# Kernel tuning notes

Measured on AMD Instinct MI355X. Metric: run time of the kernel, lower is better.

Reference implementation:

```python
import jax, jax.numpy as jnp
import numpy as np

B, C, H, W = 4, 256, 64, 64


def conv_bn_relu(x, w, b):
    # 3x3 conv, stride 1, pad 1 (SAME) + folded eval-mode BatchNorm (absorbed
    # into w, b as a per-channel affine) + ReLU.
    y = jax.lax.conv_general_dilated(
        x, w, window_strides=(1, 1), padding='SAME',
        dimension_numbers=('NCHW', 'OIHW', 'NCHW'))
    return jax.nn.relu(y + b[None, :, None, None])


def setup_inputs() -> dict:
    key = jax.random.key(0)
    ks = jax.random.split(key, 9)

    def wgt(k):
        return (jax.random.normal(k, (C, C, 3, 3), jnp.float32) * 0.02)

    def bias(k):
        return (jax.random.normal(jax.random.fold_in(k, 1), (C,), jnp.float32) * 0.02)

    return {
        'x': jax.random.normal(ks[0], (B, C, H, W), jnp.float32),
        'wq': wgt(ks[1]), 'bq': bias(ks[1]),
        'wk': wgt(ks[2]), 'bk': bias(ks[2]),
        'wv': wgt(ks[3]), 'bv': bias(ks[3]),
        'wo': wgt(ks[4]), 'bo': bias(ks[4]),
    }


def reference(x, wq, bq, wk, bk, wv, bv, wo, bo):
    b, c, h, w = x.shape
    n = h * w
    # gen_attmap: conv-BN-ReLU projections, flatten spatial dims
    q = conv_bn_relu(x, wq, bq).reshape(b, c, n)   # [B, C, N]
    k = conv_bn_relu(x, wk, bk).reshape(b, c, n)   # [B, C, N]
    v = conv_bn_relu(x, wv, bv).reshape(b, c, n)   # [B, C, N]
    # sim_map = softmax(Q^T K) over keys; context = sim_map @ V^T
    sim = jax.nn.softmax(jnp.einsum('bcn,bcm->bnm', q, k), axis=-1)  # [B, N, N]
    ctx = jnp.einsum('bnm,bcm->bcn', sim, v).reshape(b, c, h, w)
    # sub_factor == 1: the block-rearranged branch and the avg-pooled branch
    # are identical (rearrange, avgpool(1,1) and interpolate(scale=1) are all
    # identity), so x_div + x_avg == 2 * ctx.
    return conv_bn_relu(ctx + ctx, wo, bo)
```

## Files before the change

### kernel.cpp

```cpp
#include <hip/hip_runtime.h>
#include <hip/hip_fp16.h>
#include <math.h>

#define NN 4096
#define CC 256

typedef __attribute__((ext_vector_type(8))) short bf16x8;
typedef __attribute__((ext_vector_type(8))) _Float16 f16x8;
typedef __attribute__((ext_vector_type(4))) float f32x4;
typedef __attribute__((ext_vector_type(16))) float f32x16;
typedef __attribute__((ext_vector_type(8))) unsigned short u16x8;
typedef __attribute__((ext_vector_type(4))) unsigned short u16x4;
typedef __attribute__((ext_vector_type(4))) unsigned int u32x4;

__device__ inline unsigned short f2bf(float f) {
  unsigned u = __float_as_uint(f);
  return (unsigned short)((u + 0x7FFFu + ((u >> 16) & 1u)) >> 16);
}
__device__ inline float bf2f(unsigned short u) {
  return __uint_as_float(((unsigned)u) << 16);
}
__device__ inline unsigned short f2h(float f) {
  __half h = __float2half(f);
  return static_cast<__half_raw>(h).x;
}

__device__ inline void gload16(const void* g, void* l) {
  __builtin_amdgcn_global_load_lds(
      (const __attribute__((address_space(1))) void*)g,
      (__attribute__((address_space(3))) void*)l, 16, 0, 0);
}

__global__ __launch_bounds__(256) void prep_w(
    const float* __restrict__ w0, const float* __restrict__ w1,
    const float* __restrict__ w2, const float* __restrict__ w3,
    unsigned short* __restrict__ wT2, unsigned short* __restrict__ zp)
{
  int bx = blockIdx.x;
  int widx = bx >> 8;
  const float* src = (widx == 0) ? w0 : (widx == 1) ? w1 : (widx == 2) ? w2 : w3;
  int p = ((bx & 255) << 8) + threadIdx.x;
  unsigned short* dst = wT2 + (size_t)widx * 589824;
  const float* s9 = src + (size_t)p * 9;
#pragma unroll
  for (int s = 0; s < 9; ++s) dst[(size_t)s * 65536 + p] = f2bf(s9[s]);
  if (bx == 0 && threadIdx.x < 128) zp[threadIdx.x] = 0;
}

__global__ __launch_bounds__(256) void prep_x(
    const float* __restrict__ x, unsigned short* __restrict__ xT)
{
  __shared__ unsigned short T[64][72];
  int tid = threadIdx.x, bx = blockIdx.x;
  int b = bx >> 8, c0 = ((bx >> 6) & 3) * 64, n0 = (bx & 63) * 64;
#pragma unroll
  for (int it = 0; it < 16; ++it) {
    int c_l = (tid >> 6) + it * 4;
    int n_l = tid & 63;
    T[n_l][c_l] = f2bf(x[((size_t)(b * 256 + c0 + c_l)) * 4096 + n0 + n_l]);
  }
  __syncthreads();
#pragma unroll
  for (int it = 0; it < 8; ++it) {
    int n_l = (tid >> 5) + it * 8;
    int cp = (tid & 31) * 2;
    unsigned v = (unsigned)T[n_l][cp] | ((unsigned)T[n_l][cp + 1] << 16);
    *(unsigned*)&xT[((size_t)(b * 4096 + n0 + n_l)) * 256 + c0 + cp] = v;
  }
}

__global__ __launch_bounds__(256) void conv_mfma(
    const unsigned short* __restrict__ A,
    const unsigned short* __restrict__ W,
    const float* __restrict__ bias,
    void* __restrict__ out, int mode,
    const unsigned short* __restrict__ zp)
{
  __shared__ unsigned short As[2][128 * 64];
  __shared__ unsigned short Bs[2][64 * 64];

  const int tid = threadIdx.x;
  const int lane = tid & 63;
  const int w = tid >> 6;
  const int wr = w >> 1, wc = w & 1;
  const int nt = blockIdx.x & 3;
  const int mt = blockIdx.x >> 2;
  const int m0 = mt * 128;
  const int co0 = nt * 64;

  const int aslot = (lane & 7) ^ (lane >> 3);
  int gmj[4], yj[4], xj[4];
#pragma unroll
  for (int j = 0; j < 4; ++j) {
    int row = w * 32 + j * 8 + (lane >> 3);
    int gm = m0 + row;
    gmj[j] = gm;
    int n = gm & (NN - 1);
    yj[j] = n >> 6;
    xj[j] = n & 63;
  }
  int browj[2];
#pragma unroll
  for (int j = 0; j < 2; ++j)
    browj[j] = co0 + w * 16 + j * 8 + (lane >> 3);

  f32x4 acc[4][2];
#pragma unroll
  for (int mi = 0; mi < 4; ++mi)
#pragma unroll
    for (int ni = 0; ni < 2; ++ni) acc[mi][ni] = (f32x4){0.f, 0.f, 0.f, 0.f};

  auto stage = [&](int step, int sb) {
    int s = step >> 2, t = step & 3;
    int dy = s / 3 - 1, dx = s - (s / 3) * 3 - 1;
    const unsigned short* abase = A + t * 64 + aslot * 8;
    const unsigned short* wbase = W + ((size_t)s << 16) + t * 64 + aslot * 8;
#pragma unroll
    for (int j = 0; j < 4; ++j) {
      int yy = yj[j] + dy, xx = xj[j] + dx;
      bool valid = ((unsigned)yy < 64u) && ((unsigned)xx < 64u);
      const void* ga = valid
          ? (const void*)(abase + (size_t)(gmj[j] + dy * 64 + dx) * 256)
          : (const void*)zp;
      gload16(ga, (void*)&As[sb][(w * 4 + j) * 512]);
    }
#pragma unroll
    for (int j = 0; j < 2; ++j) {
      const void* gb = (const void*)(wbase + (size_t)browj[j] * 256);
      gload16(gb, (void*)&Bs[sb][(w * 2 + j) * 512]);
    }
  };

  const int r = lane & 15;
  const int klane = lane >> 4;
  const int rs = r & 7;

  int buf = 0;
  stage(0, 0);
  __syncthreads();
  for (int step = 0; step < 36; ++step) {
    if (step + 1 < 36) stage(step + 1, buf ^ 1);
    const unsigned short* as = As[buf];
    const unsigned short* bs = Bs[buf];
#pragma unroll
    for (int kk = 0; kk < 2; ++kk) {
      int slot = (kk * 4 + klane) ^ rs;
      bf16x8 a[4], bq[2];
#pragma unroll
      for (int mi = 0; mi < 4; ++mi)
        a[mi] = *(const bf16x8*)&as[(wr * 64 + mi * 16 + r) * 64 + slot * 8];
#pragma unroll
      for (int ni = 0; ni < 2; ++ni)
        bq[ni] = *(const bf16x8*)&bs[(wc * 32 + ni * 16 + r) * 64 + slot * 8];
#pragma unroll
      for (int mi = 0; mi < 4; ++mi)
#pragma unroll
        for (int ni = 0; ni < 2; ++ni)
          acc[mi][ni] = __builtin_amdgcn_mfma_f32_16x16x32_bf16(
              a[mi], bq[ni], acc[mi][ni], 0, 0, 0);
    }
    __syncthreads();
    buf ^= 1;
  }

  const int r4 = lane >> 4;
  const int colb = lane & 15;
  if (mode == 0) {
    unsigned short* o16 = (unsigned short*)out;
#pragma unroll
    for (int ni = 0; ni < 2; ++ni) {
      int co = co0 + wc * 32 + ni * 16 + colb;
      float bv = bias[co];
#pragma unroll
      for (int mi = 0; mi < 4; ++mi) {
        int gm0 = m0 + wr * 64 + mi * 16 + r4 * 4;
#pragma unroll
        for (int rr = 0; rr < 4; ++rr) {
          float v = fmaxf(acc[mi][ni][rr] + bv, 0.f);
          o16[(size_t)(gm0 + rr) * 256 + co] = f2h(v);
        }
      }
    }
  } else if (mode == 1) {
    float* o32 = (float*)out;
#pragma unroll
    for (int ni = 0; ni < 2; ++ni) {
      int co = co0 + wc * 32 + ni * 16 + colb;
      float bv = bias[co];
#pragma unroll
      for (int mi = 0; mi < 4; ++mi) {
        int gm0 = m0 + wr * 64 + mi * 16 + r4 * 4;
#pragma unroll
        for (int rr = 0; rr < 4; ++rr) {
          float v = fmaxf(acc[mi][ni][rr] + bv, 0.f);
          int gm = gm0 + rr;
          int b = gm >> 12, n = gm & (NN - 1);
          o32[((size_t)(b * 256 + co)) * 4096 + n] = v;
        }
      }
    }
  } else {
    unsigned short* o16 = (unsigned short*)out;
#pragma unroll
    for (int ni = 0; ni < 2; ++ni) {
      int co = co0 + wc * 32 + ni * 16 + colb;
      float bv = bias[co];
#pragma unroll
      for (int mi = 0; mi < 4; ++mi) {
        int gm0 = m0 + wr * 64 + mi * 16 + r4 * 4;
#pragma unroll
        for (int rr = 0; rr < 4; ++rr) {
          float v = fmaxf(acc[mi][ni][rr] + bv, 0.f);
          int gm = gm0 + rr;
          int b = gm >> 12, n = gm & (NN - 1);
          o16[((size_t)(b * 256 + co)) * 4096 + n] = f2h(v);
        }
      }
    }
  }
}

__global__ __launch_bounds__(256, 2) void attn_k(
    const unsigned short* __restrict__ qT, const unsigned short* __restrict__ kT,
    const unsigned short* __restrict__ vTc,
    unsigned short* __restrict__ pO, float2* __restrict__ pml)
{
  __shared__ unsigned short Ks[2][32 * 256];
  __shared__ unsigned short Vts[2][256 * 32];

  const int tid = threadIdx.x;
  const int lane = tid & 63;
  const int w = tid >> 6;
  const int wq = w >> 1, wc = w & 1;
  const int hi = lane >> 5;
  const int la = lane & 31;
  const int a7 = la & 7;
  const int bx = blockIdx.x;
  const int half = bx >> 8;
  const int b = (bx >> 6) & 3;
  const int q0 = (bx & 63) << 6;
  const int kbase = half << 11;

  f16x8 qf[16];
  {
    const unsigned short* qp =
        qT + ((size_t)(b * NN) + q0 + 32 * wq + la) * CC + 8 * hi;
#pragma unroll
    for (int ks = 0; ks < 16; ++ks)
      qf[ks] = *(const f16x8*)(qp + ks * 16);
  }

  const unsigned short* kTb = kT + (size_t)b * NN * CC;
  const unsigned short* vTb = vTc + (size_t)b * CC * NN;
  auto stageKV = [&](int t, int sb) {
    int k0 = kbase + (t << 5);
    {
      int row_l = lane >> 5;
      int slot = lane & 31;
#pragma unroll
      for (int i = 0; i < 4; ++i) {
        int row = 8 * w + i * 2 + row_l;
        const void* src = (const void*)(kTb + (size_t)(k0 + row) * CC +
                                        ((slot ^ (row & 7)) << 3));
        gload16(src, (void*)&Ks[sb][(8 * w + i * 2) * 256]);
      }
    }
    {
      int c_l = lane >> 2;
      int sp = lane & 3;
#pragma unroll
      for (int i = 0; i < 4; ++i) {
        int c = 64 * w + 16 * i + c_l;
        const void* src = (const void*)(vTb + (size_t)c * NN + k0 +
                                        ((sp ^ ((c >> 2) & 3)) << 3));
        gload16(src, (void*)&Vts[sb][(64 * w + 16 * i) * 32]);
      }
    }
  };

  float mprev = -INFINITY, lsum = 0.f;
  f32x16 O[4];
#pragma unroll
  for (int nc = 0; nc < 4; ++nc)
#pragma unroll
    for (int rr = 0; rr < 16; ++rr) O[nc][rr] = 0.f;

  stageKV(0, 0);
  __syncthreads();

  int buf = 0;
  for (int t = 0; t < 64; ++t) {
    if (t + 1 < 64) stageKV(t + 1, buf ^ 1);

    f32x16 S0;
#pragma unroll
    for (int rr = 0; rr < 16; ++rr) S0[rr] = 0.f;
    const unsigned short* ks_ = Ks[buf];
    __builtin_amdgcn_s_setprio(1);
#pragma unroll
    for (int ks = 0; ks < 16; ++ks) {
      f16x8 a0 = *(const f16x8*)&ks_[la * 256 + ((((ks << 1) + hi) ^ a7) << 3)];
      S0 = __builtin_amdgcn_mfma_f32_32x32x16_f16(a0, qf[ks], S0, 0, 0, 0);
    }
    __builtin_amdgcn_s_setprio(0);

    float mloc = S0[0];
#pragma unroll
    for (int rr = 1; rr < 16; ++rr) mloc = fmaxf(mloc, S0[rr]);
    {
      auto sw = __builtin_amdgcn_permlane32_swap(
          __float_as_uint(mloc), __float_as_uint(mloc), false, false);
      mloc = fmaxf(__uint_as_float(sw[0]), __uint_as_float(sw[1]));
    }
    if (!__all(mloc <= mprev + 8.f)) {
      float mnew = fmaxf(mprev, mloc);
      float sc = __expf(mprev - mnew);
      lsum *= sc;
#pragma unroll
      for (int nc = 0; nc < 4; ++nc)
#pragma unroll
        for (int rr = 0; rr < 16; ++rr) O[nc][rr] *= sc;
      mprev = mnew;
    }
    float rsm = 0.f;
#pragma unroll
    for (int rr = 0; rr < 16; ++rr) {
      S0[rr] = __expf(S0[rr] - mprev);
      rsm += S0[rr];
    }
    {
      auto sw = __builtin_amdgcn_permlane32_swap(
          __float_as_uint(rsm), __float_as_uint(rsm), false, false);
      rsm = __uint_as_float(sw[0]) + __uint_as_float(sw[1]);
    }
    lsum += rsm;

    f16x8 pf[2];
#pragma unroll
    for (int kk = 0; kk < 2; ++kk) {
      const int r0 = kk * 8;
      unsigned w0 = __builtin_bit_cast(unsigned,
          __builtin_amdgcn_cvt_pkrtz(S0[r0 + 0], S0[r0 + 1]));
      unsigned w1 = __builtin_bit_cast(unsigned,
          __builtin_amdgcn_cvt_pkrtz(S0[r0 + 2], S0[r0 + 3]));
      unsigned w2 = __builtin_bit_cast(unsigned,
          __builtin_amdgcn_cvt_pkrtz(S0[r0 + 4], S0[r0 + 5]));
      unsigned w3 = __builtin_bit_cast(unsigned,
          __builtin_amdgcn_cvt_pkrtz(S0[r0 + 6], S0[r0 + 7]));
      auto sA = __builtin_amdgcn_permlane32_swap(w0, w2, false, false);
      auto sB = __builtin_amdgcn_permlane32_swap(w1, w3, false, false);
      u32x4 fw;
      fw[0] = sA[0]; fw[1] = sB[0]; fw[2] = sA[1]; fw[3] = sB[1];
      pf[kk] = __builtin_bit_cast(f16x8, fw);
    }

    const unsigned short* vs_ = Vts[buf];
    __builtin_amdgcn_s_setprio(1);
#pragma unroll
    for (int kk = 0; kk < 2; ++kk) {
#pragma unroll
      for (int nc = 0; nc < 4; ++nc) {
        int c = 128 * wc + 32 * nc + la;
        f16x8 vf = *(const f16x8*)&vs_[c * 32 +
                                       ((((kk << 1) + hi) ^ ((c >> 2) & 3)) << 3)];
        O[nc] = __builtin_amdgcn_mfma_f32_32x32x16_f16(vf, pf[kk], O[nc], 0, 0, 0);
      }
    }
    __builtin_amdgcn_s_setprio(0);

    __syncthreads();
    buf ^= 1;
  }

  {
    int n = q0 + 32 * wq + la;
    unsigned short* dst = pO + (((size_t)(half * 4 + b)) * NN + n) * CC;
#pragma unroll
    for (int nc = 0; nc < 4; ++nc) {
#pragma unroll
      for (int tq = 0; tq < 4; ++tq) {
        int c0 = 128 * wc + 32 * nc + 8 * tq + 4 * hi;
        u16x4 pk;
        pk[0] = f2bf(O[nc][4 * tq + 0]);
        pk[1] = f2bf(O[nc][4 * tq + 1]);
        pk[2] = f2bf(O[nc][4 * tq + 2]);
        pk[3] = f2bf(O[nc][4 * tq + 3]);
        *(u16x4*)&dst[c0] = pk;
      }
    }
    if (wc == 0 && hi == 0)
      pml[(size_t)half * 4 * NN + (size_t)b * NN + n] =
          make_float2(mprev, lsum);
  }
}

__global__ __launch_bounds__(256) void combine_k(
    const unsigned short* __restrict__ pO, const float2* __restrict__ pml,
    unsigned short* __restrict__ ctx)
{
  int bx = blockIdx.x;
  int b = bx >> 6;
  int q = ((bx & 63) << 6) + (threadIdx.x >> 2);
  int c0 = (threadIdx.x & 3) << 6;
  size_t nidx = (size_t)b * NN + q;
  float2 ml0 = pml[nidx];
  float2 ml1 = pml[(size_t)4 * NN + nidx];
  float m = fmaxf(ml0.x, ml1.x);
  float w0 = __expf(ml0.x - m), w1 = __expf(ml1.x - m);
  float inv = 2.f / (ml0.y * w0 + ml1.y * w1);
  const unsigned short* p0 = pO + nidx * CC + c0;
  const unsigned short* p1 = pO + (size_t)4 * NN * CC + nidx * CC + c0;
  unsigned short* d = ctx + nidx * CC + c0;
#pragma unroll
  for (int j = 0; j < 8; ++j) {
    u16x8 a = *(const u16x8*)(p0 + j * 8);
    u16x8 bb = *(const u16x8*)(p1 + j * 8);
    u16x8 o;
#pragma unroll
    for (int e = 0; e < 8; ++e)
      o[e] = f2bf((bf2f(a[e]) * w0 + bf2f(bb[e]) * w1) * inv);
    *(u16x8*)(d + j * 8) = o;
  }
}

extern "C" void kernel_launch(void* const* d_in, const int* in_sizes, int n_in,
                              void* d_out, int out_size, void* d_ws, size_t ws_size,
                              hipStream_t stream) {
  const float* x  = (const float*)d_in[0];
  const float* wq = (const float*)d_in[1];
  const float* bq = (const float*)d_in[2];
  const float* wk = (const float*)d_in[3];
  const float* bk = (const float*)d_in[4];
  const float* wv = (const float*)d_in[5];
  const float* bv = (const float*)d_in[6];
  const float* wo = (const float*)d_in[7];
  const float* bo = (const float*)d_in[8];

  char* ws = (char*)d_ws;
  unsigned short* xT  = (unsigned short*)(ws);
  unsigned short* wT2 = (unsigned short*)(ws + 8388608);
  unsigned short* qT  = (unsigned short*)(ws + 13107200);
  unsigned short* kT  = (unsigned short*)(ws + 21495808);
  unsigned short* vTc = (unsigned short*)(ws + 29884416);
  unsigned short* ctx = (unsigned short*)(ws + 38273024);
  unsigned short* zp  = (unsigned short*)(ws + 46661632);
  unsigned short* pO  = (unsigned short*)(ws + 46662144);
  float2*         pml = (float2*)(ws + 63439360);

  prep_w<<<dim3(1024), 256, 0, stream>>>(wq, wk, wv, wo, wT2, zp);
  prep_x<<<dim3(1024), 256, 0, stream>>>(x, xT);
  conv_mfma<<<dim3(512), 256, 0, stream>>>(xT, wT2,               bq, qT, 0, zp);
  conv_mfma<<<dim3(512), 256, 0, stream>>>(xT, wT2 + 589824,      bk, kT, 0, zp);
  conv_mfma<<<dim3(512), 256, 0, stream>>>(xT, wT2 + 2 * 589824,  bv, vTc, 2, zp);
  attn_k<<<dim3(512), 256, 0, stream>>>(qT, kT, vTc, pO, pml);
  combine_k<<<dim3(256), 256, 0, stream>>>(pO, pml, ctx);
  conv_mfma<<<dim3(512), 256, 0, stream>>>(ctx, wT2 + 3 * 589824, bo, (float*)d_out, 1, zp);
}
```

Measured before the change: 298.1 us.

## Fuse QKV convs into one GEMM and split attention keys into quarters

The three Q/K/V convolutions become one implicit-GEMM kernel over a concatenated weight tensor, using 128x128 output tiles, so the input is staged once per tile instead of three times. The attention kernel splits keys into four quarters instead of two, doubling the grid. It raises launch bounds to three blocks per CU and single-buffers V using explicit vmcnt waits and raw barriers to save LDS. The combine kernel merges four partial results, reusing the xT and ctx buffers as partial storage. This adds partial-output traffic and in-place aliasing of ctx in the combine step in exchange for better CU fill and fewer launches.

```diff
diff --git a/kernel.cpp b/kernel.cpp
--- a/kernel.cpp
+++ b/kernel.cpp
@@ -13,6 +13,14 @@
 typedef __attribute__((ext_vector_type(4))) unsigned short u16x4;
 typedef __attribute__((ext_vector_type(4))) unsigned int u32x4;
 
+#define WAITVM(N) asm volatile("s_waitcnt vmcnt(" #N ")" ::: "memory")
+
+__device__ inline void hbar() {
+  __builtin_amdgcn_sched_barrier(0);
+  __builtin_amdgcn_s_barrier();
+  __builtin_amdgcn_sched_barrier(0);
+}
+
 __device__ inline unsigned short f2bf(float f) {
   unsigned u = __float_as_uint(f);
   return (unsigned short)((u + 0x7FFFu + ((u >> 16) & 1u)) >> 16);
@@ -34,17 +42,24 @@
 __global__ __launch_bounds__(256) void prep_w(
     const float* __restrict__ w0, const float* __restrict__ w1,
     const float* __restrict__ w2, const float* __restrict__ w3,
-    unsigned short* __restrict__ wT2, unsigned short* __restrict__ zp)
+    unsigned short* __restrict__ wqkv, unsigned short* __restrict__ wT2o,
+    unsigned short* __restrict__ zp)
 {
   int bx = blockIdx.x;
   int widx = bx >> 8;
   const float* src = (widx == 0) ? w0 : (widx == 1) ? w1 : (widx == 2) ? w2 : w3;
   int p = ((bx & 255) << 8) + threadIdx.x;
-  unsigned short* dst = wT2 + (size_t)widx * 589824;
   const float* s9 = src + (size_t)p * 9;
-#pragma unroll
-  for (int s = 0; s < 9; ++s) dst[(size_t)s * 65536 + p] = f2bf(s9[s]);
-  if (bx == 0 && threadIdx.x < 128) zp[threadIdx.x] = 0;
+  if (widx < 3) {
+#pragma unroll
+    for (int s = 0; s < 9; ++s)
+      wqkv[(size_t)s * 196608 + (size_t)widx * 65536 + p] = f2bf(s9[s]);
+  } else {
+#pragma unroll
+    for (int s = 0; s < 9; ++s)
+      wT2o[(size_t)s * 65536 + p] = f2bf(s9[s]);
+  }
+  if (bx == 0 && threadIdx.x < 256) zp[threadIdx.x] = 0;
 }
 
 __global__ __launch_bounds__(256) void prep_x(
@@ -69,11 +84,127 @@
   }
 }
 
+__global__ __launch_bounds__(256) void qkv_k(
+    const unsigned short* __restrict__ A,
+    const unsigned short* __restrict__ W,
+    const float* __restrict__ bq, const float* __restrict__ bk,
+    const float* __restrict__ bvv,
+    unsigned short* __restrict__ qT, unsigned short* __restrict__ kT,
+    unsigned short* __restrict__ vTc,
+    const unsigned short* __restrict__ zp)
+{
+  __shared__ unsigned short As[2][128 * 64];
+  __shared__ unsigned short Bs[2][128 * 64];
+
+  const int tid = threadIdx.x;
+  const int lane = tid & 63;
+  const int w = tid >> 6;
+  const int wr = w >> 1, wc = w & 1;
+  const int m0 = blockIdx.y * 128;
+  const int co0 = blockIdx.x * 128;
+
+  const int aslot = (lane & 7) ^ (lane >> 3);
+  int gmj[4], yj[4], xj[4], browj[4];
+#pragma unroll
+  for (int j = 0; j < 4; ++j) {
+    int row = w * 32 + j * 8 + (lane >> 3);
+    int gm = m0 + row;
+    gmj[j] = gm;
+    int n = gm & (NN - 1);
+    yj[j] = n >> 6;
+    xj[j] = n & 63;
+    browj[j] = co0 + row;
+  }
+
+  f32x4 acc[4][4];
+#pragma unroll
+  for (int mi = 0; mi < 4; ++mi)
+#pragma unroll
+    for (int ni = 0; ni < 4; ++ni) acc[mi][ni] = (f32x4){0.f, 0.f, 0.f, 0.f};
+
+  auto stage = [&](int step, int sb) {
+    int s = step >> 2, t = step & 3;
+    int dy = s / 3 - 1, dx = s - (s / 3) * 3 - 1;
+    const unsigned short* abase = A + t * 64 + aslot * 8;
+    const unsigned short* wbase = W + (size_t)s * 196608 + t * 64 + aslot * 8;
+#pragma unroll
+    for (int j = 0; j < 4; ++j) {
+      int yy = yj[j] + dy, xx = xj[j] + dx;
+      bool valid = ((unsigned)yy < 64u) && ((unsigned)xx < 64u);
+      const void* ga = valid
+          ? (const void*)(abase + (size_t)(gmj[j] + dy * 64 + dx) * 256)
+          : (const void*)zp;
+      gload16(ga, (void*)&As[sb][(w * 4 + j) * 512]);
+      const void* gb = (const void*)(wbase + (size_t)browj[j] * 256);
+      gload16(gb, (void*)&Bs[sb][(w * 4 + j) * 512]);
+    }
+  };
+
+  const int r = lane & 15;
+  const int klane = lane >> 4;
+  const int rs = r & 7;
+
+  int buf = 0;
+  stage(0, 0);
+  __syncthreads();
+  for (int step = 0; step < 36; ++step) {
+    if (step + 1 < 36) stage(step + 1, buf ^ 1);
+    const unsigned short* as = As[buf];
+    const unsigned short* bs = Bs[buf];
+#pragma unroll
+    for (int kk = 0; kk < 2; ++kk) {
+      int slot = (kk * 4 + klane) ^ rs;
+      bf16x8 a[4], bfr[4];
+#pragma unroll
+      for (int mi = 0; mi < 4; ++mi)
+        a[mi] = *(const bf16x8*)&as[(wr * 64 + mi * 16 + r) * 64 + slot * 8];
+#pragma unroll
+      for (int ni = 0; ni < 4; ++ni)
+        bfr[ni] = *(const bf16x8*)&bs[(wc * 64 + ni * 16 + r) * 64 + slot * 8];
+#pragma unroll
+      for (int mi = 0; mi < 4; ++mi)
+#pragma unroll
+        for (int ni = 0; ni < 4; ++ni)
+          acc[mi][ni] = __builtin_amdgcn_mfma_f32_16x16x32_bf16(
+              a[mi], bfr[ni], acc[mi][ni], 0, 0, 0);
+    }
+    __syncthreads();
+    buf ^= 1;
+  }
+
+  const int tgt = co0 >> 8;
+  unsigned short* outp = (tgt == 0) ? qT : (tgt == 1) ? kT : vTc;
+  const float* bp = (tgt == 0) ? bq : (tgt == 1) ? bk : bvv;
+  const int r4 = lane >> 4;
+  const int colb = lane & 15;
+#pragma unroll
+  for (int ni = 0; ni < 4; ++ni) {
+    int cog = co0 + wc * 64 + ni * 16 + colb;
+    int col = cog & 255;
+    float bv_ = bp[col];
+#pragma unroll
+    for (int mi = 0; mi < 4; ++mi) {
+      int gm0 = m0 + wr * 64 + mi * 16 + r4 * 4;
+#pragma unroll
+      for (int rr = 0; rr < 4; ++rr) {
+        float v = fmaxf(acc[mi][ni][rr] + bv_, 0.f);
+        int gm = gm0 + rr;
+        if (tgt < 2) {
+          outp[(size_t)gm * 256 + col] = f2h(v);
+        } else {
+          int b = gm >> 12, n = gm & (NN - 1);
+          outp[((size_t)(b * 256 + col)) * 4096 + n] = f2h(v);
+        }
+      }
+    }
+  }
+}
+
 __global__ __launch_bounds__(256) void conv_mfma(
     const unsigned short* __restrict__ A,
     const unsigned short* __restrict__ W,
     const float* __restrict__ bias,
-    void* __restrict__ out, int mode,
+    float* __restrict__ out,
     const unsigned short* __restrict__ zp)
 {
   __shared__ unsigned short As[2][128 * 64];
@@ -145,19 +276,19 @@
 #pragma unroll
     for (int kk = 0; kk < 2; ++kk) {
       int slot = (kk * 4 + klane) ^ rs;
-      bf16x8 a[4], bq[2];
+      bf16x8 a[4], bfr[2];
 #pragma unroll
       for (int mi = 0; mi < 4; ++mi)
         a[mi] = *(const bf16x8*)&as[(wr * 64 + mi * 16 + r) * 64 + slot * 8];
 #pragma unroll
       for (int ni = 0; ni < 2; ++ni)
-        bq[ni] = *(const bf16x8*)&bs[(wc * 32 + ni * 16 + r) * 64 + slot * 8];
+        bfr[ni] = *(const bf16x8*)&bs[(wc * 32 + ni * 16 + r) * 64 + slot * 8];
 #pragma unroll
       for (int mi = 0; mi < 4; ++mi)
 #pragma unroll
         for (int ni = 0; ni < 2; ++ni)
           acc[mi][ni] = __builtin_amdgcn_mfma_f32_16x16x32_bf16(
-              a[mi], bq[ni], acc[mi][ni], 0, 0, 0);
+              a[mi], bfr[ni], acc[mi][ni], 0, 0, 0);
     }
     __syncthreads();
     buf ^= 1;
@@ -165,68 +296,33 @@
 
   const int r4 = lane >> 4;
   const int colb = lane & 15;
-  if (mode == 0) {
-    unsigned short* o16 = (unsigned short*)out;
-#pragma unroll
-    for (int ni = 0; ni < 2; ++ni) {
-      int co = co0 + wc * 32 + ni * 16 + colb;
-      float bv = bias[co];
-#pragma unroll
-      for (int mi = 0; mi < 4; ++mi) {
-        int gm0 = m0 + wr * 64 + mi * 16 + r4 * 4;
-#pragma unroll
-        for (int rr = 0; rr < 4; ++rr) {
-          float v = fmaxf(acc[mi][ni][rr] + bv, 0.f);
-          o16[(size_t)(gm0 + rr) * 256 + co] = f2h(v);
-        }
+#pragma unroll
+  for (int ni = 0; ni < 2; ++ni) {
+    int co = co0 + wc * 32 + ni * 16 + colb;
+    float bv = bias[co];
+#pragma unroll
+    for (int mi = 0; mi < 4; ++mi) {
+      int gm0 = m0 + wr * 64 + mi * 16 + r4 * 4;
+#pragma unroll
+      for (int rr = 0; rr < 4; ++rr) {
+        float v = fmaxf(acc[mi][ni][rr] + bv, 0.f);
+        int gm = gm0 + rr;
+        int b = gm >> 12, n = gm & (NN - 1);
+        out[((size_t)(b * 256 + co)) * 4096 + n] = v;
       }
     }
-  } else if (mode == 1) {
-    float* o32 = (float*)out;
-#pragma unroll
-    for (int ni = 0; ni < 2; ++ni) {
-      int co = co0 + wc * 32 + ni * 16 + colb;
-      float bv = bias[co];
-#pragma unroll
-      for (int mi = 0; mi < 4; ++mi) {
-        int gm0 = m0 + wr * 64 + mi * 16 + r4 * 4;
-#pragma unroll
-        for (int rr = 0; rr < 4; ++rr) {
-          float v = fmaxf(acc[mi][ni][rr] + bv, 0.f);
-          int gm = gm0 + rr;
-          int b = gm >> 12, n = gm & (NN - 1);
-          o32[((size_t)(b * 256 + co)) * 4096 + n] = v;
-        }
-      }
-    }
-  } else {
-    unsigned short* o16 = (unsigned short*)out;
-#pragma unroll
-    for (int ni = 0; ni < 2; ++ni) {
-      int co = co0 + wc * 32 + ni * 16 + colb;
-      float bv = bias[co];
-#pragma unroll
-      for (int mi = 0; mi < 4; ++mi) {
-        int gm0 = m0 + wr * 64 + mi * 16 + r4 * 4;
-#pragma unroll
-        for (int rr = 0; rr < 4; ++rr) {
-          float v = fmaxf(acc[mi][ni][rr] + bv, 0.f);
-          int gm = gm0 + rr;
-          int b = gm >> 12, n = gm & (NN - 1);
-          o16[((size_t)(b * 256 + co)) * 4096 + n] = f2h(v);
-        }
-      }
-    }
-  }
-}
-
-__global__ __launch_bounds__(256, 2) void attn_k(
+  }
+}
+
+__global__ __launch_bounds__(256, 3) void attn_k(
     const unsigned short* __restrict__ qT, const unsigned short* __restrict__ kT,
     const unsigned short* __restrict__ vTc,
-    unsigned short* __restrict__ pO, float2* __restrict__ pml)
+    unsigned short* __restrict__ pA, unsigned short* __restrict__ pB,
+    unsigned short* __restrict__ pC, unsigned short* __restrict__ pD,
+    float2* __restrict__ pml)
 {
   __shared__ unsigned short Ks[2][32 * 256];
-  __shared__ unsigned short Vts[2][256 * 32];
+  __shared__ unsigned short Vts[256 * 32];
 
   const int tid = threadIdx.x;
   const int lane = tid & 63;
@@ -236,10 +332,10 @@
   const int la = lane & 31;
   const int a7 = la & 7;
   const int bx = blockIdx.x;
-  const int half = bx >> 8;
+  const int quarter = bx >> 8;
   const int b = (bx >> 6) & 3;
   const int q0 = (bx & 63) << 6;
-  const int kbase = half << 11;
+  const int kbase = quarter << 10;
 
   f16x8 qf[16];
   {
@@ -252,29 +348,29 @@
 
   const unsigned short* kTb = kT + (size_t)b * NN * CC;
   const unsigned short* vTb = vTc + (size_t)b * CC * NN;
-  auto stageKV = [&](int t, int sb) {
+
+  auto stageK = [&](int t, int sb) {
     int k0 = kbase + (t << 5);
-    {
-      int row_l = lane >> 5;
-      int slot = lane & 31;
-#pragma unroll
-      for (int i = 0; i < 4; ++i) {
-        int row = 8 * w + i * 2 + row_l;
-        const void* src = (const void*)(kTb + (size_t)(k0 + row) * CC +
-                                        ((slot ^ (row & 7)) << 3));
-        gload16(src, (void*)&Ks[sb][(8 * w + i * 2) * 256]);
-      }
-    }
-    {
-      int c_l = lane >> 2;
-      int sp = lane & 3;
-#pragma unroll
-      for (int i = 0; i < 4; ++i) {
-        int c = 64 * w + 16 * i + c_l;
-        const void* src = (const void*)(vTb + (size_t)c * NN + k0 +
-                                        ((sp ^ ((c >> 2) & 3)) << 3));
-        gload16(src, (void*)&Vts[sb][(64 * w + 16 * i) * 32]);
-      }
+    int row_l = lane >> 5;
+    int slot = lane & 31;
+#pragma unroll
+    for (int i = 0; i < 4; ++i) {
+      int row = 8 * w + i * 2 + row_l;
+      gload16((const void*)(kTb + (size_t)(k0 + row) * CC +
+                            ((slot ^ (row & 7)) << 3)),
+              (void*)&Ks[sb][(8 * w + i * 2) * 256]);
+    }
+  };
+  auto stageV = [&](int t) {
+    int k0 = kbase + (t << 5);
+    int c_l = lane >> 2;
+    int sp = lane & 3;
+#pragma unroll
+    for (int i = 0; i < 4; ++i) {
+      int c = 64 * w + 16 * i + c_l;
+      gload16((const void*)(vTb + (size_t)c * NN + k0 +
+                            ((sp ^ ((c >> 2) & 3)) << 3)),
+              (void*)&Vts[(64 * w + 16 * i) * 32]);
     }
   };
 
@@ -285,17 +381,19 @@
 #pragma unroll
     for (int rr = 0; rr < 16; ++rr) O[nc][rr] = 0.f;
 
-  stageKV(0, 0);
-  __syncthreads();
-
-  int buf = 0;
-  for (int t = 0; t < 64; ++t) {
-    if (t + 1 < 64) stageKV(t + 1, buf ^ 1);
+  stageK(0, 0);
+  WAITVM(0);
+  hbar();
+
+  for (int t = 0; t < 32; ++t) {
+    const int cur = t & 1;
+    stageV(t);
+    if (t < 31) stageK(t + 1, cur ^ 1);
 
     f32x16 S0;
 #pragma unroll
     for (int rr = 0; rr < 16; ++rr) S0[rr] = 0.f;
-    const unsigned short* ks_ = Ks[buf];
+    const unsigned short* ks_ = Ks[cur];
     __builtin_amdgcn_s_setprio(1);
 #pragma unroll
     for (int ks = 0; ks < 16; ++ks) {
@@ -354,27 +452,31 @@
       pf[kk] = __builtin_bit_cast(f16x8, fw);
     }
 
-    const unsigned short* vs_ = Vts[buf];
+    if (t < 31) { WAITVM(4); } else { WAITVM(0); }
+    hbar();
+
     __builtin_amdgcn_s_setprio(1);
 #pragma unroll
     for (int kk = 0; kk < 2; ++kk) {
 #pragma unroll
       for (int nc = 0; nc < 4; ++nc) {
         int c = 128 * wc + 32 * nc + la;
-        f16x8 vf = *(const f16x8*)&vs_[c * 32 +
+        f16x8 vf = *(const f16x8*)&Vts[c * 32 +
                                        ((((kk << 1) + hi) ^ ((c >> 2) & 3)) << 3)];
         O[nc] = __builtin_amdgcn_mfma_f32_32x32x16_f16(vf, pf[kk], O[nc], 0, 0, 0);
       }
     }
     __builtin_amdgcn_s_setprio(0);
 
-    __syncthreads();
-    buf ^= 1;
+    WAITVM(0);
+    hbar();
   }
 
   {
     int n = q0 + 32 * wq + la;
-    unsigned short* dst = pO + (((size_t)(half * 4 + b)) * NN + n) * CC;
+    unsigned short* pOq = (quarter == 0) ? pA : (quarter == 1) ? pB
+                        : (quarter == 2) ? pC : pD;
+    unsigned short* dst = pOq + ((size_t)b * NN + n) * CC;
 #pragma unroll
     for (int nc = 0; nc < 4; ++nc) {
 #pragma unroll
@@ -389,37 +491,41 @@
       }
     }
     if (wc == 0 && hi == 0)
-      pml[(size_t)half * 4 * NN + (size_t)b * NN + n] =
-          make_float2(mprev, lsum);
+      pml[((size_t)quarter * 4 + b) * NN + n] = make_float2(mprev, lsum);
   }
 }
 
 __global__ __launch_bounds__(256) void combine_k(
-    const unsigned short* __restrict__ pO, const float2* __restrict__ pml,
-    unsigned short* __restrict__ ctx)
+    const unsigned short* __restrict__ p0, const unsigned short* __restrict__ p1,
+    const unsigned short* __restrict__ p2, const unsigned short* __restrict__ p3,
+    const float2* __restrict__ pml, unsigned short* __restrict__ ctx)
 {
   int bx = blockIdx.x;
-  int b = bx >> 6;
-  int q = ((bx & 63) << 6) + (threadIdx.x >> 2);
-  int c0 = (threadIdx.x & 3) << 6;
-  size_t nidx = (size_t)b * NN + q;
-  float2 ml0 = pml[nidx];
-  float2 ml1 = pml[(size_t)4 * NN + nidx];
-  float m = fmaxf(ml0.x, ml1.x);
+  int b = bx >> 7;
+  int q = ((bx & 127) << 5) + (threadIdx.x >> 3);
+  int c0 = (threadIdx.x & 7) << 5;
+  size_t nq = (size_t)b * NN + q;
+  float2 ml0 = pml[(size_t)(0 * 4 + b) * NN + q];
+  float2 ml1 = pml[(size_t)(1 * 4 + b) * NN + q];
+  float2 ml2 = pml[(size_t)(2 * 4 + b) * NN + q];
+  float2 ml3 = pml[(size_t)(3 * 4 + b) * NN + q];
+  float m = fmaxf(fmaxf(ml0.x, ml1.x), fmaxf(ml2.x, ml3.x));
   float w0 = __expf(ml0.x - m), w1 = __expf(ml1.x - m);
-  float inv = 2.f / (ml0.y * w0 + ml1.y * w1);
-  const unsigned short* p0 = pO + nidx * CC + c0;
-  const unsigned short* p1 = pO + (size_t)4 * NN * CC + nidx * CC + c0;
-  unsigned short* d = ctx + nidx * CC + c0;
-#pragma unroll
-  for (int j = 0; j < 8; ++j) {
-    u16x8 a = *(const u16x8*)(p0 + j * 8);
-    u16x8 bb = *(const u16x8*)(p1 + j * 8);
+  float w2 = __expf(ml2.x - m), w3 = __expf(ml3.x - m);
+  float inv = 2.f / (ml0.y * w0 + ml1.y * w1 + ml2.y * w2 + ml3.y * w3);
+  size_t base = nq * CC + c0;
+#pragma unroll
+  for (int j = 0; j < 4; ++j) {
+    u16x8 a0 = *(const u16x8*)(p0 + base + j * 8);
+    u16x8 a1 = *(const u16x8*)(p1 + base + j * 8);
+    u16x8 a2 = *(const u16x8*)(p2 + base + j * 8);
+    u16x8 a3 = *(const u16x8*)(p3 + base + j * 8);
     u16x8 o;
 #pragma unroll
     for (int e = 0; e < 8; ++e)
-      o[e] = f2bf((bf2f(a[e]) * w0 + bf2f(bb[e]) * w1) * inv);
-    *(u16x8*)(d + j * 8) = o;
+      o[e] = f2bf((bf2f(a0[e]) * w0 + bf2f(a1[e]) * w1 +
+                   bf2f(a2[e]) * w2 + bf2f(a3[e]) * w3) * inv);
+    *(u16x8*)(ctx + base + j * 8) = o;
   }
 }
 
@@ -437,22 +543,22 @@
   const float* bo = (const float*)d_in[8];
 
   char* ws = (char*)d_ws;
-  unsigned short* xT  = (unsigned short*)(ws);
-  unsigned short* wT2 = (unsigned short*)(ws + 8388608);
-  unsigned short* qT  = (unsigned short*)(ws + 13107200);
-  unsigned short* kT  = (unsigned short*)(ws + 21495808);
-  unsigned short* vTc = (unsigned short*)(ws + 29884416);
-  unsigned short* ctx = (unsigned short*)(ws + 38273024);
-  unsigned short* zp  = (unsigned short*)(ws + 46661632);
-  unsigned short* pO  = (unsigned short*)(ws + 46662144);
-  float2*         pml = (float2*)(ws + 63439360);
-
-  prep_w<<<dim3(1024), 256, 0, stream>>>(wq, wk, wv, wo, wT2, zp);
+  unsigned short* xT   = (unsigned short*)(ws);
+  unsigned short* wqkv = (unsigned short*)(ws + 8388608);
+  unsigned short* wT2o = (unsigned short*)(ws + 11927552);
+  unsigned short* qT   = (unsigned short*)(ws + 13107200);
+  unsigned short* kT   = (unsigned short*)(ws + 21495808);
+  unsigned short* vTc  = (unsigned short*)(ws + 29884416);
+  unsigned short* ctx  = (unsigned short*)(ws + 38273024);
+  unsigned short* zp   = (unsigned short*)(ws + 46661632);
+  unsigned short* pO2  = (unsigned short*)(ws + 46662144);
+  unsigned short* pO3  = (unsigned short*)(ws + 55050752);
+  float2*         pml  = (float2*)(ws + 63439360);
+
+  prep_w<<<dim3(1024), 256, 0, stream>>>(wq, wk, wv, wo, wqkv, wT2o, zp);
   prep_x<<<dim3(1024), 256, 0, stream>>>(x, xT);
-  conv_mfma<<<dim3(512), 256, 0, stream>>>(xT, wT2,               bq, qT, 0, zp);
-  conv_mfma<<<dim3(512), 256, 0, stream>>>(xT, wT2 + 589824,      bk, kT, 0, zp);
-  conv_mfma<<<dim3(512), 256, 0, stream>>>(xT, wT2 + 2 * 589824,  bv, vTc, 2, zp);
-  attn_k<<<dim3(512), 256, 0, stream>>>(qT, kT, vTc, pO, pml);
-  combine_k<<<dim3(256), 256, 0, stream>>>(pO, pml, ctx);
-  conv_mfma<<<dim3(512), 256, 0, stream>>>(ctx, wT2 + 3 * 589824, bo, (float*)d_out, 1, zp);
-}
+  qkv_k<<<dim3(6, 128), 256, 0, stream>>>(xT, wqkv, bq, bk, bv, qT, kT, vTc, zp);
+  attn_k<<<dim3(1024), 256, 0, stream>>>(qT, kT, vTc, xT, ctx, pO2, pO3, pml);
+  combine_k<<<dim3(512), 256, 0, stream>>>(xT, ctx, pO2, pO3, pml, ctx);
+  conv_mfma<<<dim3(512), 256, 0, stream>>>(ctx, wT2o, bo, (float*)d_out, zp);
+}
```

Result: slower. 442.6 us (+48.5%).
